# Performance work log

Measured on AMD Instinct MI355X. Metric: run time of the kernel, lower is better.

## Reference

```python
import jax, jax.numpy as jnp
import numpy as np

H, D = 4, 32
HID = H * D  # 128
NA, NW, NO = 100_000, 20_000, 50_000
E = 150_000
OFFS = (0, NA, NA + NW, NA + NW + NO)
NTOT = OFFS[3]
# node order: assignments=0, workers=1, orders=2
# edge types (src_type, dst_type): w->a, o->a, a->w, a->o
ETYPES = ((1, 0), (2, 0), (0, 1), (0, 2))


def setup_inputs() -> dict:
    key = jax.random.key(0)
    ks = jax.random.split(key, 20)
    s = 0.05
    return {
        "x_a": jax.random.normal(ks[0], (NA, 64), jnp.float32),
        "x_w": jax.random.normal(ks[1], (NW, 64), jnp.float32),
        "x_o": jax.random.normal(ks[2], (NO, 64), jnp.float32),
        "W_in": jax.random.normal(ks[3], (3, 64, HID), jnp.float32) * s,
        "b_in": jnp.zeros((3, HID), jnp.float32),
        "W_kqv": jax.random.normal(ks[4], (2, 3, HID, 3 * HID), jnp.float32) * s,
        "b_kqv": jnp.zeros((2, 3, 3 * HID), jnp.float32),
        "a_rel": jax.random.normal(ks[5], (2, 4, H, D, D), jnp.float32) * s,
        "m_rel": jax.random.normal(ks[6], (2, 4, H, D, D), jnp.float32) * s,
        "p_rel": jnp.ones((2, 4, H), jnp.float32),
        "skip_p": jnp.ones((2, 3), jnp.float32),
        "W_o": jax.random.normal(ks[7], (2, 3, HID, HID), jnp.float32) * s,
        "b_o": jnp.zeros((2, 3, HID), jnp.float32),
        "ln_g": jnp.ones((2, 3, HID), jnp.float32),
        "ln_b": jnp.zeros((2, 3, HID), jnp.float32),
        "w_head": jax.random.normal(ks[8], (HID, 1), jnp.float32) * s,
        "b_head": jnp.zeros((1,), jnp.float32),
        "base": jnp.zeros((1,), jnp.float32),
        "src_wa": jax.random.randint(ks[9], (E,), 0, NW),
        "dst_wa": jax.random.randint(ks[10], (E,), 0, NA),
        "src_oa": jax.random.randint(ks[11], (E,), 0, NO),
        "dst_oa": jax.random.randint(ks[12], (E,), 0, NA),
        "src_aw": jax.random.randint(ks[13], (E,), 0, NA),
        "dst_aw": jax.random.randint(ks[14], (E,), 0, NW),
        "src_ao": jax.random.randint(ks[15], (E,), 0, NA),
        "dst_ao": jax.random.randint(ks[16], (E,), 0, NO),
    }


def _ln(x, g, b):
    mu = jnp.mean(x, axis=-1, keepdims=True)
    var = jnp.var(x, axis=-1, keepdims=True)
    return (x - mu) * jax.lax.rsqrt(var + 1e-5) * g + b


def _hgt_forward(x_a, x_w, x_o, W_in, b_in, W_kqv, b_kqv, a_rel, m_rel, p_rel,
                 skip_p, W_o, b_o, ln_g, ln_b, w_head, b_head, base, edges):
    # input projection + relu per node type
    xs = [jax.nn.relu(x @ W_in[t] + b_in[t]) for t, x in enumerate((x_a, x_w, x_o))]
    scale = 1.0 / np.sqrt(D).astype(np.float32)
    for l in range(2):  # num_layers (structurally distinct params)
        # per-node-type fused K/Q/V projection (PyG kqv_lin)
        kqv = [xs[t] @ W_kqv[l, t] + b_kqv[l, t] for t in range(3)]
        kd = [m[:, :HID].reshape(-1, H, D) for m in kqv]
        qd = [m[:, HID:2 * HID].reshape(-1, H, D) for m in kqv]
        vd = [m[:, 2 * HID:].reshape(-1, H, D) for m in kqv]
        alphas, vals, dsts = [], [], []
        for e, (st, dt) in enumerate(ETYPES):  # 4 relation types
            src, dst = edges[e]
            # per-edge-type per-head relation transforms applied at node level
            ke = jnp.einsum('nhd,hde->nhe', kd[st], a_rel[l, e])
            ve = jnp.einsum('nhd,hde->nhe', vd[st], m_rel[l, e])
            kg = ke[src]            # [E,H,D] gather
            vg = ve[src]
            qg = qd[dt][dst]
            alphas.append((qg * kg).sum(-1) * p_rel[l, e] * scale)  # [E,H]
            vals.append(vg)
            dsts.append(OFFS[dt] + dst)
        alpha = jnp.concatenate(alphas, axis=0)   # [Etot,H]
        vall = jnp.concatenate(vals, axis=0)      # [Etot,H,D]
        dstg = jnp.concatenate(dsts, axis=0)      # [Etot]
        # segment softmax over all incoming edges of each destination node
        amax = jax.ops.segment_max(alpha, dstg, num_segments=NTOT)
        ex = jnp.exp(alpha - amax[dstg])
        den = jax.ops.segment_sum(ex, dstg, num_segments=NTOT)
        w = ex / (den[dstg] + 1e-16)
        agg = jax.ops.segment_sum(w[:, :, None] * vall, dstg, num_segments=NTOT)
        agg = agg.reshape(NTOT, HID)
        new_xs = []
        for t in range(3):
            o = agg[OFFS[t]:OFFS[t + 1]]
            o = jax.nn.gelu(o, approximate=False) @ W_o[l, t] + b_o[l, t]
            g = jax.nn.sigmoid(skip_p[l, t])
            o = g * o + (1.0 - g) * xs[t]
            new_xs.append(jax.nn.relu(_ln(o, ln_g[l, t], ln_b[l, t])))
        xs = new_xs
    delta = (xs[0] @ w_head)[:, 0] + b_head[0]
    return base[0] + delta  # [NA]


def reference(x_a, x_w, x_o, W_in, b_in, W_kqv, b_kqv, a_rel, m_rel, p_rel,
              skip_p, W_o, b_o, ln_g, ln_b, w_head, b_head, base,
              src_wa, dst_wa, src_oa, dst_oa, src_aw, dst_aw, src_ao, dst_ao):
    edges = ((src_wa, dst_wa), (src_oa, dst_oa), (src_aw, dst_aw), (src_ao, dst_ao))
    return _hgt_forward(x_a, x_w, x_o, W_in, b_in, W_kqv, b_kqv, a_rel, m_rel,
                        p_rel, skip_p, W_o, b_o, ln_g, ln_b, w_head, b_head,
                        base, edges)
```

## Files before the change

### kernel.cpp

```cpp
#include <hip/hip_runtime.h>
#include <cstddef>
#include <cmath>

namespace {

constexpr int H = 4, D = 32, HID = 128;
constexpr int NA = 100000, NW = 20000, NO = 50000;
constexpr int NTOT = NA + NW + NO;
constexpr int E = 150000;
constexpr float SCALE = 0.17677669529663687f;
constexpr int LDK = 3 * HID;

typedef __attribute__((ext_vector_type(8))) short short8v;
typedef __attribute__((ext_vector_type(4))) float f32x4;

__device__ __forceinline__ float gelu_exact(float x) {
  return 0.5f * x * (1.f + erff(x * 0.7071067811865475f));
}
__device__ __forceinline__ unsigned short f2bf(float f) {
  unsigned u = __float_as_uint(f);
  return (unsigned short)((u + 0x7FFF + ((u >> 16) & 1)) >> 16);
}
__device__ __forceinline__ float bf2f(unsigned short s) {
  return __uint_as_float(((unsigned)s) << 16);
}
__device__ __forceinline__ float blo(unsigned w) {
  return __uint_as_float(w << 16);
}
__device__ __forceinline__ float bhi(unsigned w) {
  return __uint_as_float(w & 0xFFFF0000u);
}

__device__ __forceinline__ int btype(int bx, int nb0, int nb01) {
  return bx < nb0 ? 0 : (bx < nb01 ? 1 : 2);
}

template <int KSTEPS, bool A_FP32>
__device__ __forceinline__ void gemm_body(
    const void* __restrict__ Av, int lda, const unsigned short* __restrict__ BT,
    int ldb, f32x4* acc, int M, int bm) {
  __shared__ unsigned short As[64 * 64];
  __shared__ unsigned short Bs[128 * 64];
  const int tid = threadIdx.x;
  const int wv = tid >> 6, l = tid & 63;
  for (int ks = 0; ks < KSTEPS; ks++) {
    const int kk = ks * 64;
    #pragma unroll
    for (int p = 0; p < 2; p++) {
      int idx = tid + p * 256;
      int r = idx >> 3, c = idx & 7;
      int gr = bm + r;
      unsigned short tmp[8] = {0, 0, 0, 0, 0, 0, 0, 0};
      if (gr < M) {
        if (A_FP32) {
          const float* src = (const float*)Av + (size_t)gr * lda + kk + c * 8;
          float4 f0 = *(const float4*)src;
          float4 f1 = *(const float4*)(src + 4);
          tmp[0] = f2bf(f0.x); tmp[1] = f2bf(f0.y);
          tmp[2] = f2bf(f0.z); tmp[3] = f2bf(f0.w);
          tmp[4] = f2bf(f1.x); tmp[5] = f2bf(f1.y);
          tmp[6] = f2bf(f1.z); tmp[7] = f2bf(f1.w);
        } else {
          *(uint4*)tmp = *(const uint4*)((const unsigned short*)Av +
                                         (size_t)gr * lda + kk + c * 8);
        }
      }
      *(uint4*)&As[r * 64 + ((c ^ (r & 7)) * 8)] = *(const uint4*)tmp;
    }
    #pragma unroll
    for (int p = 0; p < 4; p++) {
      int idx = tid + p * 256;
      int r = idx >> 3, c = idx & 7;
      uint4 v = *(const uint4*)(BT + (size_t)r * ldb + kk + c * 8);
      *(uint4*)&Bs[r * 64 + ((c ^ (r & 7)) * 8)] = v;
    }
    __syncthreads();
    const int arow = wv * 16 + (l & 15);
    #pragma unroll
    for (int ksub = 0; ksub < 2; ksub++) {
      int ch = ksub * 4 + (l >> 4);
      short8v af = *(const short8v*)&As[arow * 64 + ((ch ^ (arow & 7)) * 8)];
      #pragma unroll
      for (int n = 0; n < 8; n++) {
        int brow = n * 16 + (l & 15);
        short8v bf =
            *(const short8v*)&Bs[brow * 64 + ((ch ^ (brow & 7)) * 8)];
        acc[n] =
            __builtin_amdgcn_mfma_f32_16x16x32_bf16(af, bf, acc[n], 0, 0, 0);
      }
    }
    __syncthreads();
  }
}

__global__ __launch_bounds__(256) void prep_weights(
    const float* __restrict__ W_in, const float* __restrict__ W_kqv,
    const float* __restrict__ W_o, unsigned short* __restrict__ WinT,
    unsigned short* __restrict__ Wk0T, unsigned short* __restrict__ WoT) {
  int idx = blockIdx.x * 256 + threadIdx.x;
  const int N1 = 3 * 128 * 64, N2 = 2 * 384 * 128, N3 = 6 * 128 * 128;
  if (idx < N1) {
    int t = idx / 8192, rem = idx - t * 8192;
    int n = rem >> 6, k = rem & 63;
    WinT[idx] = f2bf(W_in[(size_t)t * 64 * 128 + (size_t)k * 128 + n]);
  } else if (idx < N1 + N2) {
    int r = idx - N1;
    int lyr = r / (384 * 128), rem = r - lyr * (384 * 128);
    int n = rem >> 7, k = rem & 127;
    Wk0T[r] = f2bf(W_kqv[(size_t)lyr * 3 * 128 * 384 + (size_t)k * 384 + n]);
  } else if (idx < N1 + N2 + N3) {
    int r = idx - N1 - N2;
    int lt = r / (128 * 128), rem = r - lt * (128 * 128);
    int n = rem >> 7, k = rem & 127;
    WoT[r] = f2bf(W_o[(size_t)lt * 128 * 128 + (size_t)k * 128 + n]);
  }
}

__global__ __launch_bounds__(256) void fold_weights2(
    const float* __restrict__ W_kqv, const float* __restrict__ b_kqv,
    const float* __restrict__ a_rel, const float* __restrict__ m_rel,
    unsigned short* __restrict__ WeT, float* __restrict__ be) {
  const int lyr = blockIdx.y;
  const size_t DD = (size_t)H * D * D;
  const float* Wl = W_kqv + (size_t)lyr * 3 * HID * LDK;
  const float* bl = b_kqv + (size_t)lyr * 3 * LDK;
  const float* Al = a_rel + (size_t)lyr * 4 * DD;
  const float* Ml = m_rel + (size_t)lyr * 4 * DD;
  unsigned short* WeTl = WeT + (size_t)lyr * 2 * 384 * 128;
  float* bel = be + (size_t)lyr * 2 * 384;
  int idx = blockIdx.x * 256 + threadIdx.x;
  const int NW_ = 2 * 128 * 384;
  if (idx < NW_) {
    int tt = idx / (128 * 384);
    int rem = idx - tt * (128 * 384);
    int r = rem / 384, c = rem - r * 384;
    int slice = c >> 7, h = (c >> 5) & 3, j = c & 31;
    const float* Wsrc = Wl + (size_t)(tt + 1) * 128 * 384 + (size_t)r * 384;
    float acc = 0.f;
    if (slice == 0) {
      const float* A = Al + ((size_t)tt * H + h) * D * D;
      for (int d = 0; d < 32; d++) acc += Wsrc[h * 32 + d] * A[d * 32 + j];
    } else if (slice == 1) {
      const float* A = Al + ((size_t)(2 + tt) * H + h) * D * D;
      for (int e = 0; e < 32; e++)
        acc += Wsrc[128 + h * 32 + e] * A[j * 32 + e];
    } else {
      const float* Mm = Ml + ((size_t)tt * H + h) * D * D;
      for (int d = 0; d < 32; d++)
        acc += Wsrc[256 + h * 32 + d] * Mm[d * 32 + j];
    }
    WeTl[(size_t)tt * 384 * 128 + (size_t)c * 128 + r] = f2bf(acc);
  } else if (idx < NW_ + 2 * 384) {
    int rem = idx - NW_;
    int tt = rem / 384, c = rem - tt * 384;
    int slice = c >> 7, h = (c >> 5) & 3, j = c & 31;
    const float* bsrc = bl + (size_t)(tt + 1) * 384;
    float acc = 0.f;
    if (slice == 0) {
      const float* A = Al + ((size_t)tt * H + h) * D * D;
      for (int d = 0; d < 32; d++) acc += bsrc[h * 32 + d] * A[d * 32 + j];
    } else if (slice == 1) {
      const float* A = Al + ((size_t)(2 + tt) * H + h) * D * D;
      for (int e = 0; e < 32; e++)
        acc += bsrc[128 + h * 32 + e] * A[j * 32 + e];
    } else {
      const float* Mm = Ml + ((size_t)tt * H + h) * D * D;
      for (int d = 0; d < 32; d++)
        acc += bsrc[256 + h * 32 + d] * Mm[d * 32 + j];
    }
    bel[rem] = acc;
  }
}

__global__ __launch_bounds__(256) void in_fused(
    const float* __restrict__ xa, const float* __restrict__ xw,
    const float* __restrict__ xo, const unsigned short* __restrict__ WinT,
    const float* __restrict__ b_in, unsigned short* __restrict__ xs, int nb0,
    int nb01) {
  int t = btype(blockIdx.x, nb0, nb01);
  int base = t == 0 ? 0 : (t == 1 ? nb0 : nb01);
  int M = t == 0 ? NA : (t == 1 ? NW : NO);
  int off = t == 0 ? 0 : (t == 1 ? NA : NA + NW);
  const float* A = t == 0 ? xa : (t == 1 ? xw : xo);
  const int bm = (blockIdx.x - base) * 64;
  f32x4 acc[8] = {};
  gemm_body<1, true>(A, 64, WinT + (size_t)t * 128 * 64, 64, acc, M, bm);
  const int l = threadIdx.x & 63, wv = threadIdx.x >> 6;
  const float* bias = b_in + t * HID;
  unsigned short* C = xs + (size_t)off * HID;
  #pragma unroll
  for (int n = 0; n < 8; n++) {
    int col = n * 16 + (l & 15);
    float bb = bias[col];
    #pragma unroll
    for (int j = 0; j < 4; j++) {
      int row = bm + wv * 16 + (l >> 4) * 4 + j;
      if (row < M) C[(size_t)row * HID + col] = f2bf(fmaxf(acc[n][j] + bb, 0.f));
    }
  }
}

__global__ __launch_bounds__(256) void kqv_fused(
    const unsigned short* __restrict__ xs, const unsigned short* __restrict__ Wk0Tl,
    const float* __restrict__ b0, const unsigned short* __restrict__ WeT,
    const float* __restrict__ be, unsigned short* __restrict__ kqvB, int nb0,
    int nb01) {
  int t = btype(blockIdx.x, nb0, nb01);
  int base = t == 0 ? 0 : (t == 1 ? nb0 : nb01);
  int M = t == 0 ? NA : (t == 1 ? NW : NO);
  int off = t == 0 ? 0 : (t == 1 ? NA : NA + NW);
  const unsigned short* BT =
      (t == 0 ? Wk0Tl : WeT + (size_t)(t - 1) * 384 * 128);
  const float* bias = t == 0 ? b0 : be + (size_t)(t - 1) * 384;
  const int bm = (blockIdx.x - base) * 64;
  const int bn = blockIdx.y * 128;
  f32x4 acc[8] = {};
  gemm_body<2, false>(xs + (size_t)off * HID, HID, BT + (size_t)bn * 128, 128,
                      acc, M, bm);
  const int l = threadIdx.x & 63, wv = threadIdx.x >> 6;
  unsigned short* C = kqvB + (size_t)off * LDK;
  #pragma unroll
  for (int n = 0; n < 8; n++) {
    int col = bn + n * 16 + (l & 15);
    float bb = bias[col];
    #pragma unroll
    for (int j = 0; j < 4; j++) {
      int row = bm + wv * 16 + (l >> 4) * 4 + j;
      if (row < M) C[(size_t)row * LDK + col] = f2bf(acc[n][j] + bb);
    }
  }
}

__global__ __launch_bounds__(256) void wo_ln_fused(
    const unsigned short* __restrict__ kqvB, const unsigned short* __restrict__ WoTl,
    const float* __restrict__ bl, unsigned short* __restrict__ xs,
    const float* __restrict__ skipl, const float* __restrict__ gll,
    const float* __restrict__ bll, int nb0, int nb01) {
  int t = btype(blockIdx.x, nb0, nb01);
  int base = t == 0 ? 0 : (t == 1 ? nb0 : nb01);
  int M = t == 0 ? NA : (t == 1 ? NW : NO);
  int off = t == 0 ? 0 : (t == 1 ? NA : NA + NW);
  const int bm = (blockIdx.x - base) * 64;
  f32x4 acc[8] = {};
  gemm_body<2, false>(kqvB + (size_t)off * LDK + HID, LDK,
                      WoTl + (size_t)t * 128 * 128, 128, acc, M, bm);
  const int l = threadIdx.x & 63, wv = threadIdx.x >> 6;
  const float* bias = bl + t * HID;
  const float* gln = gll + t * HID;
  const float* bln = bll + t * HID;
  unsigned short* xsT = xs + (size_t)off * HID;
  const float g = 1.f / (1.f + expf(-skipl[t]));
  float bb[8], gl8[8], bl8[8];
  #pragma unroll
  for (int n = 0; n < 8; n++) {
    int col = n * 16 + (l & 15);
    bb[n] = bias[col];
    gl8[n] = gln[col];
    bl8[n] = bln[col];
  }
  #pragma unroll
  for (int j = 0; j < 4; j++) {
    int row = bm + wv * 16 + (l >> 4) * 4 + j;
    bool ok = row < M;
    float vv[8], sum = 0.f, sq = 0.f;
    #pragma unroll
    for (int n = 0; n < 8; n++) {
      int col = n * 16 + (l & 15);
      float xo = ok ? bf2f(xsT[(size_t)row * HID + col]) : 0.f;
      float val = g * (acc[n][j] + bb[n]) + (1.f - g) * xo;
      vv[n] = val;
      sum += val;
      sq += val * val;
    }
    #pragma unroll
    for (int m = 1; m < 16; m <<= 1) {
      sum += __shfl_xor(sum, m, 64);
      sq += __shfl_xor(sq, m, 64);
    }
    float mu = sum * (1.f / 128.f);
    float var = sq * (1.f / 128.f) - mu * mu;
    float r = rsqrtf(var + 1e-5f);
    if (ok) {
      #pragma unroll
      for (int n = 0; n < 8; n++) {
        float y = fmaxf((vv[n] - mu) * r * gl8[n] + bl8[n], 0.f);
        xsT[(size_t)row * HID + n * 16 + (l & 15)] = f2bf(y);
      }
    }
  }
}

__global__ __launch_bounds__(256) void csr_hist4(
    const int* __restrict__ d0, const int* __restrict__ d1,
    const int* __restrict__ d2, const int* __restrict__ d3,
    int* __restrict__ cnt) {
  int t = blockIdx.x * 256 + threadIdx.x;
  if (t >= 4 * E) return;
  int et = t / E, e = t - et * E;
  const int* dp = et == 0 ? d0 : et == 1 ? d1 : et == 2 ? d2 : d3;
  int base = et == 0 ? 0 : et == 1 ? NA : et == 2 ? 2 * NA : 2 * NA + NW;
  atomicAdd(&cnt[base + dp[e]], 1);
}

__global__ __launch_bounds__(256) void scan_block_all(
    const int* __restrict__ cnt, int* __restrict__ rpAll,
    int* __restrict__ bsum) {
  const int nbA = (NA + 255) / 256, nbW = (NW + 255) / 256,
            nbO = (NO + 255) / 256;
  int bx = blockIdx.x;
  int et, bbase, cbase, rpo, n;
  if (bx < nbA) { et = 0; bbase = 0; cbase = 0; rpo = 0; n = NA; }
  else if (bx < 2 * nbA) { et = 1; bbase = nbA; cbase = NA; rpo = NA + 1; n = NA; }
  else if (bx < 2 * nbA + nbW) {
    et = 2; bbase = 2 * nbA; cbase = 2 * NA; rpo = 2 * (NA + 1); n = NW;
  } else {
    et = 3; bbase = 2 * nbA + nbW; cbase = 2 * NA + NW;
    rpo = 2 * (NA + 1) + (NW + 1); n = NO;
  }
  int lb = bx - bbase;
  __shared__ int tmp[256];
  int i = lb * 256 + threadIdx.x;
  int v = (i < n) ? cnt[cbase + i] : 0;
  tmp[threadIdx.x] = v;
  __syncthreads();
  int acc = v;
  for (int off = 1; off < 256; off <<= 1) {
    int other = (threadIdx.x >= off) ? tmp[threadIdx.x - off] : 0;
    __syncthreads();
    acc += other;
    tmp[threadIdx.x] = acc;
    __syncthreads();
  }
  if (i < n) rpAll[rpo + i] = acc - v;
  if (threadIdx.x == 255) bsum[et * 512 + lb] = acc;
}

__global__ __launch_bounds__(256) void scan_bsums_all(int* __restrict__ bsum) {
  int et = blockIdx.x;
  int nb = et < 2 ? (NA + 255) / 256 : (et == 2 ? (NW + 255) / 256
                                                : (NO + 255) / 256);
  int* bs = bsum + et * 512;
  __shared__ int tmp[256];
  __shared__ int carry;
  if (threadIdx.x == 0) carry = 0;
  __syncthreads();
  for (int start = 0; start < nb; start += 256) {
    int i = start + threadIdx.x;
    int v = (i < nb) ? bs[i] : 0;
    tmp[threadIdx.x] = v;
    __syncthreads();
    int acc = v;
    for (int off = 1; off < 256; off <<= 1) {
      int other = (threadIdx.x >= off) ? tmp[threadIdx.x - off] : 0;
      __syncthreads();
      acc += other;
      tmp[threadIdx.x] = acc;
      __syncthreads();
    }
    int c = carry;
    if (i < nb) bs[i] = c + acc - v;
    __syncthreads();
    if (threadIdx.x == 255) carry = c + acc;
    __syncthreads();
  }
}

__device__ __forceinline__ void et_of_node(int i, int& et, int& base, int& nd,
                                           int& rpo) {
  if (i < NA) { et = 0; base = 0; nd = NA; rpo = 0; }
  else if (i < 2 * NA) { et = 1; base = NA; nd = NA; rpo = NA + 1; }
  else if (i < 2 * NA + NW) { et = 2; base = 2 * NA; nd = NW; rpo = 2 * (NA + 1); }
  else { et = 3; base = 2 * NA + NW; nd = NO; rpo = 2 * (NA + 1) + NW + 1; }
}

__global__ __launch_bounds__(256) void csr_finalize4(
    int* __restrict__ rpAll, const int* __restrict__ bsum,
    int* __restrict__ cursor) {
  int i = blockIdx.x * 256 + threadIdx.x;
  if (i >= 2 * NA + NW + NO) return;
  int et, base, nd, rpo;
  et_of_node(i, et, base, nd, rpo);
  int local = i - base;
  int v = rpAll[rpo + local] + bsum[et * 512 + (local >> 8)];
  rpAll[rpo + local] = v;
  cursor[base + local] = v;
  if (local == 0) rpAll[rpo + nd] = E;
}

__global__ __launch_bounds__(256) void csr_scatter4(
    const int* __restrict__ d0, const int* __restrict__ d1,
    const int* __restrict__ d2, const int* __restrict__ d3,
    int* __restrict__ cursor, int* __restrict__ ceAll) {
  int t = blockIdx.x * 256 + threadIdx.x;
  if (t >= 4 * E) return;
  int et = t / E, e = t - et * E;
  const int* dp = et == 0 ? d0 : et == 1 ? d1 : et == 2 ? d2 : d3;
  int base = et == 0 ? 0 : et == 1 ? NA : et == 2 ? 2 * NA : 2 * NA + NW;
  int slot = atomicAdd(&cursor[base + dp[e]], 1);
  ceAll[(size_t)et * E + slot] = e;
}

__global__ __launch_bounds__(256) void csr_sort4(const int* __restrict__ rpAll,
                                                 int* __restrict__ ceAll) {
  int i = blockIdx.x * 256 + threadIdx.x;
  if (i >= 2 * NA + NW + NO) return;
  int et, base, nd, rpo;
  et_of_node(i, et, base, nd, rpo);
  int local = i - base;
  int b = rpAll[rpo + local], e = rpAll[rpo + local + 1];
  int* ce = ceAll + (size_t)et * E;
  for (int k = b + 1; k < e; k++) {
    int key = ce[k];
    int j = k - 1;
    while (j >= b && ce[j] > key) { ce[j + 1] = ce[j]; j--; }
    ce[j + 1] = key;
  }
}

__global__ __launch_bounds__(256) void build_sd(
    const int* __restrict__ ce, const int* __restrict__ s0,
    const int* __restrict__ s1, const int* __restrict__ s2,
    const int* __restrict__ s3, int* __restrict__ srcOf) {
  int t = blockIdx.x * 256 + threadIdx.x;
  if (t >= 4 * E) return;
  int et = t / E;
  int e = ce[t];
  const int* sp = et == 0 ? s0 : et == 1 ? s1 : et == 2 ? s2 : s3;
  int sOff = et == 0 ? NA : et == 1 ? NA + NW : 0;
  srcOf[t] = sOff + sp[e];
}

__global__ __launch_bounds__(256) void build_desc(const int* __restrict__ rpAll,
                                                  int4* __restrict__ desc) {
  int dl = blockIdx.x * 256 + threadIdx.x;
  if (dl >= NTOT) return;
  int4 d;
  if (dl < NA) {
    d.x = rpAll[dl]; d.y = rpAll[dl + 1];
    d.z = rpAll[(NA + 1) + dl]; d.w = rpAll[(NA + 1) + dl + 1];
  } else if (dl < NA + NW) {
    int x = dl - NA;
    d.x = rpAll[2 * (NA + 1) + x]; d.y = rpAll[2 * (NA + 1) + x + 1];
    d.z = 0; d.w = 0;
  } else {
    int x = dl - NA - NW;
    d.x = rpAll[2 * (NA + 1) + (NW + 1) + x];
    d.y = rpAll[2 * (NA + 1) + (NW + 1) + x + 1];
    d.z = 0; d.w = 0;
  }
  desc[dl] = d;
}

__global__ __launch_bounds__(256) void attn_fused(
    const unsigned short* __restrict__ kqv, const int4* __restrict__ desc,
    const int* __restrict__ srcOf, const float* __restrict__ Pl,
    const float* __restrict__ Ml, unsigned short* __restrict__ out) {
  int dl = (blockIdx.x * 256 + threadIdx.x) >> 6;
  int lane = threadIdx.x & 63;
  if (dl >= NTOT) return;
  int q = lane >> 4, p = lane & 15;
  int4 dd = desc[dl];
  int b0 = dd.x, e0 = dd.y, b1 = dd.z, e1 = dd.w;
  int et23 = -1;
  const int* so0;
  const int* so1 = srcOf;
  float ps0, ps1 = 0.f;
  if (dl < NA) {
    so0 = srcOf; so1 = srcOf + E;
    ps0 = Pl[q] * SCALE; ps1 = Pl[H + q] * SCALE;
  } else if (dl < NA + NW) {
    so0 = srcOf + 2 * (size_t)E;
    ps0 = Pl[2 * H + q] * SCALE;
    et23 = 2;
  } else {
    so0 = srcOf + 3 * (size_t)E;
    ps0 = Pl[3 * H + q] * SCALE;
    et23 = 3;
  }
  const int n0 = e0 - b0;
  const int n01 = n0 + (e1 - b1);
  auto srcAt = [&](int t) -> int {
    return (t < n0) ? so0[b0 + t] : so1[b1 + (t - n0)];
  };
  unsigned qv = *(const unsigned*)(kqv + (size_t)dl * LDK + HID + lane * 2);
  float qx = blo(qv), qy = bhi(qv);
  const int lo2 = lane * 2;

  float m = -INFINITY, den = 0.f, ax = 0.f, ay = 0.f;
  unsigned ka = 0, va = 0, kb = 0, vb = 0;
  int i2 = 0, i3 = 0;
  if (n01 > 0) {
    const unsigned short* r = kqv + (size_t)srcAt(0) * LDK;
    ka = *(const unsigned*)(r + lo2);
    va = *(const unsigned*)(r + 2 * HID + lo2);
  }
  if (n01 > 1) {
    const unsigned short* r = kqv + (size_t)srcAt(1) * LDK;
    kb = *(const unsigned*)(r + lo2);
    vb = *(const unsigned*)(r + 2 * HID + lo2);
  }
  if (n01 > 2) i2 = srcAt(2);
  if (n01 > 3) i3 = srcAt(3);
  int t = 0;
  for (; t + 1 < n01; t += 2) {
    unsigned pka = ka, pva = va, pkb = kb, pvb = vb;
    float psa = (t < n0) ? ps0 : ps1;
    float psb = (t + 1 < n0) ? ps0 : ps1;
    if (t + 2 < n01) {
      const unsigned short* r = kqv + (size_t)i2 * LDK;
      ka = *(const unsigned*)(r + lo2);
      va = *(const unsigned*)(r + 2 * HID + lo2);
    }
    if (t + 3 < n01) {
      const unsigned short* r = kqv + (size_t)i3 * LDK;
      kb = *(const unsigned*)(r + lo2);
      vb = *(const unsigned*)(r + 2 * HID + lo2);
    }
    if (t + 4 < n01) i2 = srcAt(t + 4);
    if (t + 5 < n01) i3 = srcAt(t + 5);
    float sa = qx * blo(pka) + qy * bhi(pka);
    float sb = qx * blo(pkb) + qy * bhi(pkb);
    sa += __shfl_xor(sa, 1, 64);
    sb += __shfl_xor(sb, 1, 64);
    sa += __shfl_xor(sa, 2, 64);
    sb += __shfl_xor(sb, 2, 64);
    sa += __shfl_xor(sa, 4, 64);
    sb += __shfl_xor(sb, 4, 64);
    sa += __shfl_xor(sa, 8, 64);
    sb += __shfl_xor(sb, 8, 64);
    sa *= psa;
    sb *= psb;
    float nm = fmaxf(m, fmaxf(sa, sb));
    float c = __expf(m - nm);
    float wa = __expf(sa - nm), wb = __expf(sb - nm);
    den = den * c + wa + wb;
    ax = ax * c + wa * blo(pva) + wb * blo(pvb);
    ay = ay * c + wa * bhi(pva) + wb * bhi(pvb);
    m = nm;
  }
  if (t < n01) {
    float ps = (t < n0) ? ps0 : ps1;
    float s = qx * blo(ka) + qy * bhi(ka);
    s += __shfl_xor(s, 1, 64);
    s += __shfl_xor(s, 2, 64);
    s += __shfl_xor(s, 4, 64);
    s += __shfl_xor(s, 8, 64);
    s *= ps;
    float nm = fmaxf(m, s);
    float c = __expf(m - nm);
    float w = __expf(s - nm);
    den = den * c + w;
    ax = ax * c + w * blo(va);
    ay = ay * c + w * bhi(va);
  }
  float inv = 1.f / (den + 1e-16f);
  ax *= inv;
  ay *= inv;
  if (et23 >= 0) {
    const float* Mm = Ml + ((size_t)et23 * H + q) * D * D;
    int base = lane & 48;
    float o0 = 0.f, o1 = 0.f;
    #pragma unroll
    for (int j = 0; j < 16; j++) {
      float s0 = __shfl(ax, base + j, 64);
      float s1 = __shfl(ay, base + j, 64);
      float2 m0 = *(const float2*)&Mm[(2 * j) * 32 + 2 * p];
      float2 m1 = *(const float2*)&Mm[(2 * j + 1) * 32 + 2 * p];
      o0 += s0 * m0.x + s1 * m1.x;
      o1 += s0 * m0.y + s1 * m1.y;
    }
    ax = o0; ay = o1;
  }
  unsigned ov = (unsigned)f2bf(gelu_exact(ax)) |
                ((unsigned)f2bf(gelu_exact(ay)) << 16);
  *(unsigned*)(out + (size_t)dl * LDK + HID + lane * 2) = ov;
}

__global__ __launch_bounds__(256) void head_kernel(
    const unsigned short* __restrict__ xs0, const float* __restrict__ w_head,
    const float* __restrict__ b_head, const float* __restrict__ basep,
    float* __restrict__ out, int Nrows) {
  int wid = (blockIdx.x * 256 + threadIdx.x) >> 6;
  int lane = threadIdx.x & 63;
  if (wid >= Nrows) return;
  size_t base = (size_t)wid * HID;
  float d = bf2f(xs0[base + lane]) * w_head[lane] +
            bf2f(xs0[base + 64 + lane]) * w_head[64 + lane];
  #pragma unroll
  for (int m = 1; m < 64; m <<= 1) d += __shfl_xor(d, m, 64);
  if (lane == 0) out[wid] = basep[0] + b_head[0] + d;
}

}

extern "C" void kernel_launch(void* const* d_in, const int* in_sizes, int n_in,
                              void* d_out, int out_size, void* d_ws,
                              size_t ws_size, hipStream_t stream) {
  const float* x_a = (const float*)d_in[0];
  const float* x_w = (const float*)d_in[1];
  const float* x_o = (const float*)d_in[2];
  const float* W_in = (const float*)d_in[3];
  const float* b_in = (const float*)d_in[4];
  const float* W_kqv = (const float*)d_in[5];
  const float* b_kqv = (const float*)d_in[6];
  const float* a_rel = (const float*)d_in[7];
  const float* m_rel = (const float*)d_in[8];
  const float* p_rel = (const float*)d_in[9];
  const float* skip_p = (const float*)d_in[10];
  const float* W_o = (const float*)d_in[11];
  const float* b_o = (const float*)d_in[12];
  const float* ln_g = (const float*)d_in[13];
  const float* ln_b = (const float*)d_in[14];
  const float* w_head = (const float*)d_in[15];
  const float* b_head = (const float*)d_in[16];
  const float* basep = (const float*)d_in[17];
  const int* srcs[4] = {(const int*)d_in[18], (const int*)d_in[20],
                        (const int*)d_in[22], (const int*)d_in[24]};
  const int* dsts[4] = {(const int*)d_in[19], (const int*)d_in[21],
                        (const int*)d_in[23], (const int*)d_in[25]};

  const size_t SZ_XS = (size_t)NTOT * HID * 2;
  const size_t SZ_KQV = (size_t)NTOT * LDK * 2;
  const size_t SZ_WINT = (size_t)3 * 128 * 64 * 2;
  const size_t SZ_WK0T = (size_t)2 * 384 * 128 * 2;
  const size_t SZ_WOT = (size_t)6 * 128 * 128 * 2;
  const size_t SZ_WET = (size_t)2 * 2 * 384 * 128 * 2;
  const size_t SZ_BE = ((size_t)2 * 2 * 384 * 4 + 63) & ~63ull;
  const size_t SZ_SD = (size_t)4 * E * 4;
  const size_t SZ_DESC = (size_t)NTOT * 16;
  const int CNT_TOT = 2 * NA + NW + NO;
  const int RP_TOT = 2 * (NA + 1) + (NW + 1) + (NO + 1);
  const size_t SZ_RP = ((size_t)RP_TOT * 4 + 63) & ~63ull;
  const size_t SZ_CE = (size_t)4 * E * 4;
  const size_t SZ_CU = ((size_t)CNT_TOT * 4 + 63) & ~63ull;
  const size_t SZ_BS = 4 * 512 * 4;
  const size_t need = SZ_XS + SZ_KQV + SZ_WINT + SZ_WK0T + SZ_WOT + SZ_WET +
                      SZ_BE + SZ_SD + SZ_DESC + SZ_RP + SZ_CE + 2 * SZ_CU +
                      SZ_BS;
  if (ws_size < need) return;

  char* p = (char*)d_ws;
  unsigned short* xs = (unsigned short*)p;    p += SZ_XS;
  unsigned short* kqvB = (unsigned short*)p;  p += SZ_KQV;
  unsigned short* WinT = (unsigned short*)p;  p += SZ_WINT;
  unsigned short* Wk0T = (unsigned short*)p;  p += SZ_WK0T;
  unsigned short* WoT = (unsigned short*)p;   p += SZ_WOT;
  unsigned short* WeT = (unsigned short*)p;   p += SZ_WET;
  float* beB = (float*)p;                     p += SZ_BE;
  int* srcOf = (int*)p;                       p += SZ_SD;
  int4* descB = (int4*)p;                     p += SZ_DESC;
  int* rpAll = (int*)p;                       p += SZ_RP;
  int* ceAll = (int*)p;                       p += SZ_CE;
  int* cursor = (int*)p;                      p += SZ_CU;
  int* cnt = (int*)p;                         p += SZ_CU;
  int* bsum = (int*)p;

  const int CNTT = 2 * NA + NW + NO;
  const int e4b = (4 * E + 255) / 256;
  const int nb0 = (NA + 63) / 64, nb01 = nb0 + (NW + 63) / 64;
  const int nbTot = nb01 + (NO + 63) / 64;
  const int nbA = (NA + 255) / 256, nbW = (NW + 255) / 256,
            nbO = (NO + 255) / 256;

  hipMemsetAsync(cnt, 0, (size_t)CNTT * 4, stream);
  csr_hist4<<<e4b, 256, 0, stream>>>(dsts[0], dsts[1], dsts[2], dsts[3], cnt);
  scan_block_all<<<2 * nbA + nbW + nbO, 256, 0, stream>>>(cnt, rpAll, bsum);
  scan_bsums_all<<<4, 256, 0, stream>>>(bsum);
  csr_finalize4<<<(CNTT + 255) / 256, 256, 0, stream>>>(rpAll, bsum, cursor);
  csr_scatter4<<<e4b, 256, 0, stream>>>(dsts[0], dsts[1], dsts[2], dsts[3],
                                        cursor, ceAll);
  csr_sort4<<<(CNTT + 255) / 256, 256, 0, stream>>>(rpAll, ceAll);
  build_sd<<<e4b, 256, 0, stream>>>(ceAll, srcs[0], srcs[1], srcs[2], srcs[3],
                                    srcOf);
  build_desc<<<(NTOT + 255) / 256, 256, 0, stream>>>(rpAll, descB);

  prep_weights<<<(3 * 128 * 64 + 2 * 384 * 128 + 6 * 128 * 128 + 255) / 256,
                 256, 0, stream>>>(W_in, W_kqv, W_o, WinT, Wk0T, WoT);
  fold_weights2<<<dim3((2 * 128 * 384 + 2 * 384 + 255) / 256, 2), 256, 0,
                  stream>>>(W_kqv, b_kqv, a_rel, m_rel, WeT, beB);
  in_fused<<<nbTot, 256, 0, stream>>>(x_a, x_w, x_o, WinT, b_in, xs, nb0, nb01);

  const size_t DD = (size_t)H * D * D;
  for (int l = 0; l < 2; l++) {
    const float* Ml = m_rel + (size_t)l * 4 * DD;
    const float* Pl = p_rel + (size_t)l * 4 * H;
    const float* bl = b_kqv + (size_t)l * 3 * LDK;
    kqv_fused<<<dim3(nbTot, 3), 256, 0, stream>>>(
        xs, Wk0T + (size_t)l * 384 * 128, bl,
        WeT + (size_t)l * 2 * 384 * 128, beB + (size_t)l * 2 * 384, kqvB, nb0,
        nb01);
    attn_fused<<<(NTOT + 3) / 4, 256, 0, stream>>>(kqvB, descB, srcOf, Pl, Ml,
                                                   kqvB);
    wo_ln_fused<<<nbTot, 256, 0, stream>>>(
        kqvB, WoT + (size_t)l * 3 * 128 * 128, b_o + (size_t)l * 3 * HID, xs,
        skip_p + l * 3, ln_g + (size_t)l * 3 * HID, ln_b + (size_t)l * 3 * HID,
        nb0, nb01);
  }
  head_kernel<<<(NA + 3) / 4, 256, 0, stream>>>(xs, w_head, b_head, basep,
                                                (float*)d_out, NA);
}
```

Baseline: 703.8 us.

## Reuse A tile across all three KQV column blocks in one kernel block

The KQV GEMM previously launched three column blocks per row tile, each reloading the same 64x128 activation tile. Now each block stages the A tile once in XOR-swizzled shared memory and loops over the three 128-column output slices, reloading only the weight tile. This cuts redundant activation reads and launches a third as many blocks. In exchange each block uses 48KB of LDS, which may lower occupancy, and the weight loads are serialized behind barriers within each block.

```diff
diff --git a/kernel.cpp b/kernel.cpp
--- a/kernel.cpp
+++ b/kernel.cpp
@@ -205,6 +205,8 @@
     const float* __restrict__ b0, const unsigned short* __restrict__ WeT,
     const float* __restrict__ be, unsigned short* __restrict__ kqvB, int nb0,
     int nb01) {
+  __shared__ unsigned short As[64 * 128];
+  __shared__ unsigned short Bs[128 * 128];
   int t = btype(blockIdx.x, nb0, nb01);
   int base = t == 0 ? 0 : (t == 1 ? nb0 : nb01);
   int M = t == 0 ? NA : (t == 1 ? NW : NO);
@@ -213,20 +215,53 @@
       (t == 0 ? Wk0Tl : WeT + (size_t)(t - 1) * 384 * 128);
   const float* bias = t == 0 ? b0 : be + (size_t)(t - 1) * 384;
   const int bm = (blockIdx.x - base) * 64;
-  const int bn = blockIdx.y * 128;
-  f32x4 acc[8] = {};
-  gemm_body<2, false>(xs + (size_t)off * HID, HID, BT + (size_t)bn * 128, 128,
-                      acc, M, bm);
-  const int l = threadIdx.x & 63, wv = threadIdx.x >> 6;
+  const int tid = threadIdx.x;
+  const int wv = tid >> 6, l = tid & 63;
+  #pragma unroll
+  for (int p = 0; p < 4; p++) {
+    int idx = tid + p * 256;
+    int r = idx >> 4, c = idx & 15;
+    int gr = bm + r;
+    uint4 v = {0, 0, 0, 0};
+    if (gr < M)
+      v = *(const uint4*)(xs + (size_t)(off + gr) * HID + c * 8);
+    *(uint4*)&As[r * 128 + ((c ^ (r & 15)) * 8)] = v;
+  }
+  const int arow = wv * 16 + (l & 15);
   unsigned short* C = kqvB + (size_t)off * LDK;
-  #pragma unroll
-  for (int n = 0; n < 8; n++) {
-    int col = bn + n * 16 + (l & 15);
-    float bb = bias[col];
-    #pragma unroll
-    for (int j = 0; j < 4; j++) {
-      int row = bm + wv * 16 + (l >> 4) * 4 + j;
-      if (row < M) C[(size_t)row * LDK + col] = f2bf(acc[n][j] + bb);
+  for (int bn = 0; bn < 384; bn += 128) {
+    if (bn) __syncthreads();
+    #pragma unroll
+    for (int p = 0; p < 8; p++) {
+      int idx = tid + p * 256;
+      int r = idx >> 4, c = idx & 15;
+      uint4 v = *(const uint4*)(BT + (size_t)(bn + r) * 128 + c * 8);
+      *(uint4*)&Bs[r * 128 + ((c ^ (r & 15)) * 8)] = v;
+    }
+    __syncthreads();
+    f32x4 acc[8] = {};
+    #pragma unroll
+    for (int ks = 0; ks < 4; ks++) {
+      int ch = ks * 4 + (l >> 4);
+      short8v af = *(const short8v*)&As[arow * 128 + ((ch ^ (arow & 15)) * 8)];
+      #pragma unroll
+      for (int n = 0; n < 8; n++) {
+        int brow = n * 16 + (l & 15);
+        short8v bf =
+            *(const short8v*)&Bs[brow * 128 + ((ch ^ (brow & 15)) * 8)];
+        acc[n] =
+            __builtin_amdgcn_mfma_f32_16x16x32_bf16(af, bf, acc[n], 0, 0, 0);
+      }
+    }
+    #pragma unroll
+    for (int n = 0; n < 8; n++) {
+      int col = bn + n * 16 + (l & 15);
+      float bb = bias[col];
+      #pragma unroll
+      for (int j = 0; j < 4; j++) {
+        int row = bm + wv * 16 + (l >> 4) * 4 + j;
+        if (row < M) C[(size_t)row * LDK + col] = f2bf(acc[n][j] + bb);
+      }
     }
   }
 }
@@ -685,7 +720,7 @@
     const float* Ml = m_rel + (size_t)l * 4 * DD;
     const float* Pl = p_rel + (size_t)l * 4 * H;
     const float* bl = b_kqv + (size_t)l * 3 * LDK;
-    kqv_fused<<<dim3(nbTot, 3), 256, 0, stream>>>(
+    kqv_fused<<<nbTot, 256, 0, stream>>>(
         xs, Wk0T + (size_t)l * 384 * 128, bl,
         WeT + (size_t)l * 2 * 384 * 128, beB + (size_t)l * 2 * 384, kqvB, nb0,
         nb01);
```

Measured after the change: 668.4 us. 1.05x faster.
